# Kernel optimization log

Hardware: AMD Instinct MI355X
Metric: run time of the kernel (lower is better)

## Reference

```python
import jax, jax.numpy as jnp
import numpy as np

DIM = 1024
NUM_HEADS = 16
HEAD_DIM = 64
SEQ_LEN = 4096
RMS_EPS = 1e-6


def rotary_tables(T, head_dim):
    # modded-nanogpt style rotary: frequencies only on first half of the half-dim,
    # second half zeroed (identity rotation).
    angular_freq = (1.0 / 1024.0) ** jnp.linspace(0.0, 1.0, head_dim // 4)
    angular_freq = jnp.concatenate([angular_freq, jnp.zeros(head_dim // 4)])
    t = jnp.arange(T, dtype=jnp.float32)
    theta = t[:, None] * angular_freq[None, :]  # [T, D/2]
    return jnp.cos(theta), jnp.sin(theta)


def apply_rotary(x, cos, sin):
    # x: [B, T, H, D]
    xf = x.astype(jnp.float32)
    x1, x2 = jnp.split(xf, 2, axis=-1)
    c = cos[None, :, None, :]
    s = sin[None, :, None, :]
    y1 = x1 * c + x2 * s
    y2 = x1 * (-s) + x2 * c
    return jnp.concatenate([y1, y2], axis=-1).astype(x.dtype)


def rms_norm(x):
    return x * jax.lax.rsqrt(jnp.mean(x * x, axis=-1, keepdims=True) + RMS_EPS)


def setup_inputs() -> dict:
    key = jax.random.key(0)
    k1, k2, k3 = jax.random.split(key, 3)
    hdim = NUM_HEADS * HEAD_DIM
    std = 0.5 * DIM ** (-0.5)
    bound = (3.0 ** 0.5) * std
    x = jax.random.normal(k1, (1, SEQ_LEN, DIM), dtype=jnp.float32)
    qkv_w = jax.random.uniform(k2, (3 * hdim, DIM), minval=-bound, maxval=bound, dtype=jnp.float32)
    # original zero-inits c_proj; use small random weights for a nontrivial baseline
    proj_w = jax.random.normal(k3, (DIM, hdim), dtype=jnp.float32) * 0.02
    lambdas = jnp.array([0.5], dtype=jnp.float32)
    return {"x": x, "qkv_w": qkv_w, "lambdas": lambdas, "proj_w": proj_w}


def reference(x, qkv_w, lambdas, proj_w):
    B, T, _ = x.shape
    H, D = NUM_HEADS, HEAD_DIM
    scale = 1.0 / (D ** 0.5)
    qkv = jnp.einsum('btc,fc->btf', x, qkv_w)            # [B, T, 3*H*D]
    qkv = qkv.reshape(B, T, 3 * H, D)
    q, k, v = jnp.split(qkv, 3, axis=-2)                  # each [B, T, H, D]
    q, k = rms_norm(q), rms_norm(k)
    cos, sin = rotary_tables(T, D)
    q, k = apply_rotary(q, cos, sin), apply_rotary(k, cos, sin)
    v = lambdas[0] * v
    scores = jnp.einsum('bqhd,bkhd->bhqk', q, k) * scale  # [B, H, T, T]
    causal = jnp.tril(jnp.ones((T, T), dtype=bool))
    scores = jnp.where(causal[None, None], scores, -jnp.inf)
    p = jax.nn.softmax(scores, axis=-1)
    y = jnp.einsum('bhqk,bkhd->bqhd', p, v)               # [B, T, H, D]
    y = y.reshape(B, T, H * D)
    return jnp.einsum('btf,cf->btc', y, proj_w)           # [B, T, DIM]
```

## Files before the change

### kernel.cpp

```cpp
#include <hip/hip_runtime.h>
#include <stdint.h>

#define SEQ 4096
#define NHEAD 16
#define HDIM 64

typedef __attribute__((ext_vector_type(4))) float f32x4;
typedef __attribute__((ext_vector_type(16))) float f32x16;
typedef __attribute__((ext_vector_type(8))) __bf16 bf16x8;
typedef __attribute__((ext_vector_type(8))) unsigned short u16x8;
typedef __attribute__((ext_vector_type(4))) unsigned short u16x4;
typedef __attribute__((ext_vector_type(4))) unsigned int u32x4;

static __device__ __forceinline__ float bf2f(unsigned short u) {
    unsigned int x = ((unsigned int)u) << 16;
    return __builtin_bit_cast(float, x);
}
static __device__ __forceinline__ unsigned short f2bf(float f) {
    unsigned int u = __builtin_bit_cast(unsigned int, f);
    u += 0x7FFFu + ((u >> 16) & 1u);
    return (unsigned short)(u >> 16);
}
static __device__ __forceinline__ f32x4 mfma_bf16_16x16x32(u16x8 a, u16x8 b, f32x4 c) {
    return __builtin_amdgcn_mfma_f32_16x16x32_bf16(
        __builtin_bit_cast(bf16x8, a), __builtin_bit_cast(bf16x8, b), c, 0, 0, 0);
}
static __device__ __forceinline__ f32x16 mfma_bf16_32x32x16(u16x8 a, u16x8 b, f32x16 c) {
    return __builtin_amdgcn_mfma_f32_32x32x16_bf16(
        __builtin_bit_cast(bf16x8, a), __builtin_bit_cast(bf16x8, b), c, 0, 0, 0);
}
static __device__ __forceinline__ void gload_lds16(const void* g, void* l) {
    __builtin_amdgcn_global_load_lds(
        (__attribute__((address_space(1))) unsigned int*)g,
        (__attribute__((address_space(3))) unsigned int*)l,
        16, 0, 0);
}
static __device__ __forceinline__ unsigned int cvtpk_bf16(float lo, float hi) {
    unsigned int r;
    asm("v_cvt_pk_bf16_f32 %0, %1, %2" : "=v"(r) : "v"(lo), "v"(hi));
    return r;
}

__global__ void cvt3_kernel(const float* __restrict__ s0, unsigned short* __restrict__ d0, int n0q,
                            const float* __restrict__ s1, unsigned short* __restrict__ d1, int n1q,
                            const float* __restrict__ s2, unsigned short* __restrict__ d2, int n2q)
{
    const int stride = gridDim.x * blockDim.x;
    const int total = n0q + n1q + n2q;
    for (int i = blockIdx.x * blockDim.x + threadIdx.x; i < total; i += stride) {
        const float* src; unsigned short* dst; int j;
        if (i < n0q)            { src = s0; dst = d0; j = i; }
        else if (i < n0q + n1q) { src = s1; dst = d1; j = i - n0q; }
        else                    { src = s2; dst = d2; j = i - n0q - n1q; }
        f32x4 v = *(const f32x4*)(src + (size_t)j * 4);
        u16x4 o;
#pragma unroll
        for (int k = 0; k < 4; k++) o[k] = f2bf(v[k]);
        *(u16x4*)(dst + (size_t)j * 4) = o;
    }
}

template<int OUT_BF16>
__global__ __launch_bounds__(256) void gemm_bt_kernel(
    const unsigned short* __restrict__ A,
    const unsigned short* __restrict__ B,
    void* __restrict__ Cv,
    int M, int N, int K, int lda)
{
    __shared__ __align__(16) unsigned short As[128 * 64];
    __shared__ __align__(16) unsigned short Bs[128 * 64];
    const int tid = threadIdx.x;
    const int lane = tid & 63;
    const int wave = tid >> 6;
    const int wm = (wave >> 1) * 64;
    const int wn = (wave & 1) * 64;
    const int bm = blockIdx.y * 128, bn = blockIdx.x * 128;
    const int l15 = lane & 15, l4 = lane >> 4;

    f32x4 acc[4][4];
#pragma unroll
    for (int i = 0; i < 4; i++)
#pragma unroll
        for (int j = 0; j < 4; j++) acc[i][j] = (f32x4){0.f, 0.f, 0.f, 0.f};

    const int srow = tid >> 3;
    const int scol = (tid & 7) * 8;
    const unsigned short* Ab = A + (size_t)(bm + srow) * lda + scol;
    const unsigned short* Bb = B + (size_t)(bn + srow) * K + scol;

    for (int kt = 0; kt < K; kt += 64) {
#pragma unroll
        for (int ci = 0; ci < 4; ci++)
            gload_lds16(Ab + (size_t)ci * 32 * lda + kt, &As[ci * 2048 + tid * 8]);
#pragma unroll
        for (int ci = 0; ci < 4; ci++)
            gload_lds16(Bb + (size_t)ci * 32 * K + kt, &Bs[ci * 2048 + tid * 8]);
        __syncthreads();
#pragma unroll
        for (int ks = 0; ks < 2; ks++) {
            const int kc = ks * 32 + l4 * 8;
            u16x8 af[4], bfr[4];
#pragma unroll
            for (int i = 0; i < 4; i++)
                af[i] = *(const u16x8*)&As[(wm + i * 16 + l15) * 64 + kc];
#pragma unroll
            for (int j = 0; j < 4; j++)
                bfr[j] = *(const u16x8*)&Bs[(wn + j * 16 + l15) * 64 + kc];
#pragma unroll
            for (int i = 0; i < 4; i++)
#pragma unroll
                for (int j = 0; j < 4; j++)
                    acc[i][j] = mfma_bf16_16x16x32(af[i], bfr[j], acc[i][j]);
        }
        __syncthreads();
    }

    const int orow = bm + wm + l4 * 4;
    const int ocol = bn + wn + l15;
#pragma unroll
    for (int i = 0; i < 4; i++)
#pragma unroll
        for (int j = 0; j < 4; j++)
#pragma unroll
            for (int r = 0; r < 4; r++) {
                size_t idx = (size_t)(orow + i * 16 + r) * N + (ocol + j * 16);
                if (OUT_BF16) ((unsigned short*)Cv)[idx] = f2bf(acc[i][j][r]);
                else          ((float*)Cv)[idx] = acc[i][j][r];
            }
}

__global__ __launch_bounds__(256) void rope_norm_tr_kernel(
    const unsigned short* __restrict__ qkv,
    const float* __restrict__ lambdas,
    unsigned short* __restrict__ qh,
    unsigned short* __restrict__ kh,
    unsigned short* __restrict__ vT)
{
    __shared__ __align__(16) unsigned short tile[64][72];
    const int h = blockIdx.x >> 6;
    const int tt = (blockIdx.x & 63) * 64;
    const int lane = threadIdx.x & 63;
    const int wave = threadIdx.x >> 6;
    const float lam = lambdas[0];
    const int i = lane & 31;
    const float w = (i < 16) ? exp2f(-(10.0f / 15.0f) * (float)i) : 0.0f;

#pragma unroll 1
    for (int it = 0; it < 16; it++) {
        const int tl = it * 4 + wave;
        const int t = tt + tl;
        const size_t base = (size_t)t * 3072 + h * 64 + lane;
        float q = bf2f(qkv[base]);
        float k = bf2f(qkv[base + 1024]);
        float v = bf2f(qkv[base + 2048]);
        float sq = q * q, sk = k * k;
#pragma unroll
        for (int m = 1; m < 64; m <<= 1) {
            sq += __shfl_xor(sq, m);
            sk += __shfl_xor(sk, m);
        }
        q *= rsqrtf(sq * (1.0f / 64.0f) + 1e-6f);
        k *= rsqrtf(sk * (1.0f / 64.0f) + 1e-6f);
        float th = (float)t * w;
        float c = cosf(th), s = sinf(th);
        float qp = __shfl_xor(q, 32);
        float kp = __shfl_xor(k, 32);
        float sg = (lane < 32) ? s : -s;
        float qo = (q * c + qp * sg) * 0.1803368801111244f;
        float ko = k * c + kp * sg;
        const size_t o = ((size_t)h * SEQ + t) * 64 + lane;
        qh[o] = f2bf(qo);
        kh[o] = f2bf(ko);
        tile[tl][lane] = f2bf(v * lam);
    }
    __syncthreads();
    const int tid = threadIdx.x;
    const int row = tid >> 2;
    const int c0 = (tid & 3) * 16;
    u16x8 o0, o1;
#pragma unroll
    for (int j = 0; j < 8; j++) { o0[j] = tile[c0 + j][row]; o1[j] = tile[c0 + 8 + j][row]; }
    u16x8* dst = (u16x8*)(vT + ((size_t)h * 64 + row) * SEQ + tt + c0);
    dst[0] = o0; dst[1] = o1;
}

__global__ __launch_bounds__(256, 2) void attn_kernel(
    const unsigned short* __restrict__ qh,
    const unsigned short* __restrict__ kh,
    const unsigned short* __restrict__ vT,
    float* __restrict__ acc,
    float* __restrict__ lacc)
{
    __shared__ __align__(16) unsigned short Ks[2][64 * 64];
    __shared__ __align__(16) unsigned short Vs[2][64 * 64];
    const int h = blockIdx.x;
    const int qp = blockIdx.y;
    const int s = blockIdx.z;
    const int tid = threadIdx.x;
    const int lane = tid & 63;
    const int wave = tid >> 6;
    const int l31 = lane & 31;
    const int hi = lane >> 5;
    const int r7 = l31 & 7;

    const unsigned short* Kb = kh + (size_t)h * SEQ * 64;
    const unsigned short* Vb = vT + (size_t)h * 64 * SEQ;

    u16x8 ones;
#pragma unroll
    for (int j = 0; j < 8; j++) ones[j] = 0x3F80;

    const int sr = tid >> 3;
    const int scs = ((tid & 7) * 8) ^ ((sr & 7) * 8);

#pragma unroll 1
    for (int ph = 0; ph < 2; ph++) {
        const int qtp = ph ? (31 - qp) : qp;
        const int nt = 2 * qtp + 2;
        const int t0 = (nt * s) >> 1;
        const int t1 = (nt * (s + 1)) >> 1;
        const int q0w = qtp * 128 + wave * 32;

        u16x8 qf[4];
        {
            const unsigned short* qb = qh + ((size_t)h * SEQ + q0w + l31) * 64 + hi * 8;
#pragma unroll
            for (int c = 0; c < 4; c++) qf[c] = *(const u16x8*)(qb + c * 16);
        }

        f32x16 o0 = {}, o1 = {}, lA = {};

        const unsigned short* kst = Kb + (size_t)(t0 * 64 + sr) * 64 + scs;
        const unsigned short* vst = Vb + (size_t)sr * SEQ + t0 * 64 + scs;

        gload_lds16(kst,            &Ks[0][tid * 8]);
        gload_lds16(kst + 32 * 64,  &Ks[0][2048 + tid * 8]);
        gload_lds16(vst,            &Vs[0][tid * 8]);
        gload_lds16(vst + 32 * SEQ, &Vs[0][2048 + tid * 8]);
        kst += 64 * 64;
        vst += 64;
        __syncthreads();

        int cur = 0;
        for (int kt = t0; kt < t1; kt++) {
            const int kv0 = kt * 64;
            if (kt + 1 < t1) {
                gload_lds16(kst,            &Ks[cur ^ 1][tid * 8]);
                gload_lds16(kst + 32 * 64,  &Ks[cur ^ 1][2048 + tid * 8]);
                gload_lds16(vst,            &Vs[cur ^ 1][tid * 8]);
                gload_lds16(vst + 32 * SEQ, &Vs[cur ^ 1][2048 + tid * 8]);
            }
            kst += 64 * 64;
            vst += 64;
            if (kv0 <= q0w + 31) {
                const unsigned short* ks0 = &Ks[cur][l31 * 64];
                const unsigned short* vs0 = &Vs[cur][l31 * 64];
                const unsigned short* ks1 = ks0 + 32 * 64;
                const unsigned short* vs1 = vs0 + 32 * 64;
                const bool half2 = (kv0 + 32 <= q0w + 31);
                const int q = q0w + l31;

                {
                    f32x16 st = {};
                    __builtin_amdgcn_s_setprio(1);
#pragma unroll
                    for (int c = 0; c < 4; c++) {
                        const int off = ((c * 2 + hi) ^ r7) * 8;
                        st = mfma_bf16_32x32x16(*(const u16x8*)(ks0 + off), qf[c], st);
                    }
                    __builtin_amdgcn_s_setprio(0);
                    asm("" : "+v"(st));
                    if (kv0 + 31 > q0w) {
#pragma unroll
                        for (int r = 0; r < 16; r++) {
                            const int crow = (r & 3) + 8 * (r >> 2) + 4 * hi;
                            if (kv0 + crow > q) st[r] = -1e30f;
                        }
                    }
#pragma unroll
                    for (int r = 0; r < 16; r++) st[r] = exp2f(st[r]);

                    u16x8 paf[2];
#pragma unroll
                    for (int kk = 0; kk < 2; kk++) {
                        const int rb = kk * 8;
                        unsigned int a0 = cvtpk_bf16(st[rb + 0], st[rb + 1]);
                        unsigned int a1 = cvtpk_bf16(st[rb + 2], st[rb + 3]);
                        unsigned int b0 = cvtpk_bf16(st[rb + 4], st[rb + 5]);
                        unsigned int b1 = cvtpk_bf16(st[rb + 6], st[rb + 7]);
                        asm("v_permlane32_swap_b32 %0, %1" : "+v"(a0), "+v"(b0));
                        asm("v_permlane32_swap_b32 %0, %1" : "+v"(a1), "+v"(b1));
                        u32x4 w;
                        w[0] = a0; w[1] = a1; w[2] = b0; w[3] = b1;
                        paf[kk] = __builtin_bit_cast(u16x8, w);
                    }
                    __builtin_amdgcn_s_setprio(1);
#pragma unroll
                    for (int kk = 0; kk < 2; kk++) {
                        const int off = ((kk * 2 + hi) ^ r7) * 8;
                        u16x8 v0 = *(const u16x8*)(vs0 + off);
                        u16x8 v1 = *(const u16x8*)(vs1 + off);
                        o0 = mfma_bf16_32x32x16(paf[kk], v0, o0);
                        o1 = mfma_bf16_32x32x16(paf[kk], v1, o1);
                        lA = mfma_bf16_32x32x16(paf[kk], ones, lA);
                    }
                    __builtin_amdgcn_s_setprio(0);
                }

                if (half2) {
                    f32x16 st = {};
                    __builtin_amdgcn_s_setprio(1);
#pragma unroll
                    for (int c = 0; c < 4; c++) {
                        const int off = ((c * 2 + hi) ^ r7) * 8;
                        st = mfma_bf16_32x32x16(*(const u16x8*)(ks1 + off), qf[c], st);
                    }
                    __builtin_amdgcn_s_setprio(0);
                    asm("" : "+v"(st));
                    if (kv0 + 63 > q0w) {
#pragma unroll
                        for (int r = 0; r < 16; r++) {
                            const int crow = (r & 3) + 8 * (r >> 2) + 4 * hi;
                            if (kv0 + 32 + crow > q) st[r] = -1e30f;
                        }
                    }
#pragma unroll
                    for (int r = 0; r < 16; r++) st[r] = exp2f(st[r]);

                    u16x8 paf[2];
#pragma unroll
                    for (int kk = 0; kk < 2; kk++) {
                        const int rb = kk * 8;
                        unsigned int a0 = cvtpk_bf16(st[rb + 0], st[rb + 1]);
                        unsigned int a1 = cvtpk_bf16(st[rb + 2], st[rb + 3]);
                        unsigned int b0 = cvtpk_bf16(st[rb + 4], st[rb + 5]);
                        unsigned int b1 = cvtpk_bf16(st[rb + 6], st[rb + 7]);
                        asm("v_permlane32_swap_b32 %0, %1" : "+v"(a0), "+v"(b0));
                        asm("v_permlane32_swap_b32 %0, %1" : "+v"(a1), "+v"(b1));
                        u32x4 w;
                        w[0] = a0; w[1] = a1; w[2] = b0; w[3] = b1;
                        paf[kk] = __builtin_bit_cast(u16x8, w);
                    }
                    __builtin_amdgcn_s_setprio(1);
#pragma unroll
                    for (int kk = 0; kk < 2; kk++) {
                        const int off = (((kk + 2) * 2 + hi) ^ r7) * 8;
                        u16x8 v0 = *(const u16x8*)(vs0 + off);
                        u16x8 v1 = *(const u16x8*)(vs1 + off);
                        o0 = mfma_bf16_32x32x16(paf[kk], v0, o0);
                        o1 = mfma_bf16_32x32x16(paf[kk], v1, o1);
                        lA = mfma_bf16_32x32x16(paf[kk], ones, lA);
                    }
                    __builtin_amdgcn_s_setprio(0);
                }
            }
            __syncthreads();
            cur ^= 1;
        }

        if (t0 * 64 <= q0w + 31) {
#pragma unroll
            for (int r = 0; r < 16; r++) {
                const int crow = (r & 3) + 8 * (r >> 2) + 4 * hi;
                float* row = acc + (size_t)(q0w + crow) * 1024 + h * 64;
                atomicAdd(row + l31,      o0[r]);
                atomicAdd(row + 32 + l31, o1[r]);
            }
            if (l31 == 0) {
#pragma unroll
                for (int r = 0; r < 16; r++) {
                    const int crow = (r & 3) + 8 * (r >> 2) + 4 * hi;
                    atomicAdd(lacc + (size_t)(q0w + crow) * 16 + h, lA[r]);
                }
            }
        }
    }
}

__global__ __launch_bounds__(256) void norm_kernel(
    const float* __restrict__ acc, const float* __restrict__ lacc,
    unsigned short* __restrict__ yb)
{
    const int i = blockIdx.x * 256 + threadIdx.x;
    const int t = i >> 8;
    const int h = (i & 255) >> 4;
    const float inv = 1.0f / lacc[t * 16 + h];
    f32x4 v = *(const f32x4*)(acc + (size_t)i * 4);
    u16x4 o;
#pragma unroll
    for (int j = 0; j < 4; j++) o[j] = f2bf(v[j] * inv);
    *(u16x4*)(yb + (size_t)i * 4) = o;
}

extern "C" void kernel_launch(void* const* d_in, const int* in_sizes, int n_in,
                              void* d_out, int out_size, void* d_ws, size_t ws_size,
                              hipStream_t stream) {
    (void)in_sizes; (void)n_in; (void)out_size; (void)ws_size;
    const float* x       = (const float*)d_in[0];
    const float* qkv_w   = (const float*)d_in[1];
    const float* lambdas = (const float*)d_in[2];
    const float* proj_w  = (const float*)d_in[3];

    char* ws = (char*)d_ws;
    unsigned short* x_bf   = (unsigned short*)(ws + 0);
    unsigned short* qkv_bf = (unsigned short*)(ws + 8388608);
    unsigned short* qh     = (unsigned short*)(ws + 33554432);
    unsigned short* kh     = (unsigned short*)(ws + 41943040);
    unsigned short* vT     = (unsigned short*)(ws + 58720256);
    unsigned short* wq_bf  = (unsigned short*)(ws + 67108864);
    unsigned short* wp_bf  = (unsigned short*)(ws + 73400320);
    unsigned short* yb     = (unsigned short*)(ws + 75497472);
    float*          acc    = (float*)(ws + 0);
    float*          lacc   = (float*)(ws + 16777216);

    cvt3_kernel<<<2048, 256, 0, stream>>>(x, x_bf, 1048576,
                                          qkv_w, wq_bf, 786432,
                                          proj_w, wp_bf, 262144);

    gemm_bt_kernel<1><<<dim3(24, 32), 256, 0, stream>>>(x_bf, wq_bf, qkv_bf, 4096, 3072, 1024, 1024);
    rope_norm_tr_kernel<<<1024, 256, 0, stream>>>(qkv_bf, lambdas, qh, kh, vT);

    hipMemsetAsync(ws, 0, 16777216 + 262144, stream);

    attn_kernel<<<dim3(16, 16, 2), 256, 0, stream>>>(qh, kh, vT, acc, lacc);
    norm_kernel<<<4096, 256, 0, stream>>>(acc, lacc, yb);

    gemm_bt_kernel<0><<<dim3(8, 32), 256, 0, stream>>>(yb, wp_bf, d_out, 4096, 1024, 1024, 1024);
}
```

Baseline: 193.8 us.

## Triple-buffer K/V tiles with explicit vmcnt waits and raw barriers

Moves the K/V staging in the attention kernel from a double buffer to a triple buffer, prefetching two tiles ahead. Full __syncthreads calls are replaced by partial s_waitcnt vmcnt(4) plus s_barrier, so the load for the tile after next stays in flight during compute. It also drops the asm register fences on the score accumulators. Shared memory per block grows from 32KB to 48KB, which may limit occupancy at two blocks per CU. The hand-counted vmcnt waits also depend on how the compiler orders the memory instructions.

```diff
diff --git a/kernel.cpp b/kernel.cpp
--- a/kernel.cpp
+++ b/kernel.cpp
@@ -191,17 +191,17 @@
     float* __restrict__ acc,
     float* __restrict__ lacc)
 {
-    __shared__ __align__(16) unsigned short Ks[2][64 * 64];
-    __shared__ __align__(16) unsigned short Vs[2][64 * 64];
+    __shared__ __align__(16) unsigned short Ks[3][64 * 64];
+    __shared__ __align__(16) unsigned short Vs[3][64 * 64];
     const int h = blockIdx.x;
     const int qp = blockIdx.y;
     const int s = blockIdx.z;
     const int tid = threadIdx.x;
     const int lane = tid & 63;
-    const int wave = tid >> 6;
     const int l31 = lane & 31;
     const int hi = lane >> 5;
     const int r7 = l31 & 7;
+    const int wave = tid >> 6;
 
     const unsigned short* Kb = kh + (size_t)h * SEQ * 64;
     const unsigned short* Vb = vT + (size_t)h * 64 * SEQ;
@@ -212,6 +212,13 @@
 
     const int sr = tid >> 3;
     const int scs = ((tid & 7) * 8) ^ ((sr & 7) * 8);
+
+#define STAGE_TILE(buf) do {                                      \
+        gload_lds16(kst,            &Ks[buf][tid * 8]);           \
+        gload_lds16(kst + 32 * 64,  &Ks[buf][2048 + tid * 8]);    \
+        gload_lds16(vst,            &Vs[buf][tid * 8]);           \
+        gload_lds16(vst + 32 * SEQ, &Vs[buf][2048 + tid * 8]);    \
+        kst += 64 * 64; vst += 64; } while (0)
 
 #pragma unroll 1
     for (int ph = 0; ph < 2; ph++) {
@@ -233,25 +240,23 @@
         const unsigned short* kst = Kb + (size_t)(t0 * 64 + sr) * 64 + scs;
         const unsigned short* vst = Vb + (size_t)sr * SEQ + t0 * 64 + scs;
 
-        gload_lds16(kst,            &Ks[0][tid * 8]);
-        gload_lds16(kst + 32 * 64,  &Ks[0][2048 + tid * 8]);
-        gload_lds16(vst,            &Vs[0][tid * 8]);
-        gload_lds16(vst + 32 * SEQ, &Vs[0][2048 + tid * 8]);
-        kst += 64 * 64;
-        vst += 64;
-        __syncthreads();
+        STAGE_TILE(0);
+        if (t0 + 1 < t1) {
+            STAGE_TILE(1);
+            asm volatile("s_waitcnt vmcnt(4)" ::: "memory");
+        } else {
+            asm volatile("s_waitcnt vmcnt(0)" ::: "memory");
+        }
+        __builtin_amdgcn_s_barrier();
 
         int cur = 0;
         for (int kt = t0; kt < t1; kt++) {
             const int kv0 = kt * 64;
-            if (kt + 1 < t1) {
-                gload_lds16(kst,            &Ks[cur ^ 1][tid * 8]);
-                gload_lds16(kst + 32 * 64,  &Ks[cur ^ 1][2048 + tid * 8]);
-                gload_lds16(vst,            &Vs[cur ^ 1][tid * 8]);
-                gload_lds16(vst + 32 * SEQ, &Vs[cur ^ 1][2048 + tid * 8]);
-            }
-            kst += 64 * 64;
-            vst += 64;
+            const bool pf = (kt + 2 < t1);
+            if (pf) {
+                int nxt = cur + 2; if (nxt >= 3) nxt -= 3;
+                STAGE_TILE(nxt);
+            }
             if (kv0 <= q0w + 31) {
                 const unsigned short* ks0 = &Ks[cur][l31 * 64];
                 const unsigned short* vs0 = &Vs[cur][l31 * 64];
@@ -269,7 +274,6 @@
                         st = mfma_bf16_32x32x16(*(const u16x8*)(ks0 + off), qf[c], st);
                     }
                     __builtin_amdgcn_s_setprio(0);
-                    asm("" : "+v"(st));
                     if (kv0 + 31 > q0w) {
 #pragma unroll
                         for (int r = 0; r < 16; r++) {
@@ -316,7 +320,6 @@
                         st = mfma_bf16_32x32x16(*(const u16x8*)(ks1 + off), qf[c], st);
                     }
                     __builtin_amdgcn_s_setprio(0);
-                    asm("" : "+v"(st));
                     if (kv0 + 63 > q0w) {
 #pragma unroll
                         for (int r = 0; r < 16; r++) {
@@ -354,9 +357,16 @@
                     __builtin_amdgcn_s_setprio(0);
                 }
             }
-            __syncthreads();
-            cur ^= 1;
-        }
+            if (pf) {
+                asm volatile("s_waitcnt vmcnt(4)" ::: "memory");
+                __builtin_amdgcn_s_barrier();
+            } else if (kt + 1 < t1) {
+                asm volatile("s_waitcnt vmcnt(0)" ::: "memory");
+                __builtin_amdgcn_s_barrier();
+            }
+            cur = (cur == 2) ? 0 : cur + 1;
+        }
+        __builtin_amdgcn_s_barrier();
 
         if (t0 * 64 <= q0w + 31) {
 #pragma unroll
@@ -375,6 +385,7 @@
             }
         }
     }
+#undef STAGE_TILE
 }
 
 __global__ __launch_bounds__(256) void norm_kernel(
```

New measurement: 196.4 us. About the same (+1.3%).
